# Kernel optimization log

Hardware: AMD Instinct MI355X
Metric: run time of the kernel (lower is better)

## Reference

```python
import jax, jax.numpy as jnp
import numpy as np

WS = (8, 8)   # window size
SS = (4, 4)   # shift size
NH = 3        # num heads


def _attn_mask(pad_H, pad_W):
    """Standard Swin shifted-window attention mask, shape (nW, L, L)."""
    img = np.zeros((pad_H, pad_W), dtype=np.int32)
    cnt = 0
    for hs in (slice(0, -WS[0]), slice(-WS[0], -SS[0]), slice(-SS[0], None)):
        for ws_ in (slice(0, -WS[1]), slice(-WS[1], -SS[1]), slice(-SS[1], None)):
            img[hs, ws_] = cnt
            cnt += 1
    nH, nW = pad_H // WS[0], pad_W // WS[1]
    m = img.reshape(nH, WS[0], nW, WS[1]).transpose(0, 2, 1, 3).reshape(nH * nW, WS[0] * WS[1])
    diff = m[:, None, :] - m[:, :, None]
    return jnp.asarray(np.where(diff != 0, -100.0, 0.0).astype(np.float32))


def setup_inputs() -> dict:
    key = jax.random.key(0)
    ks = jax.random.split(key, 6)
    B, H, W, C = 16, 128, 128, 96
    L = WS[0] * WS[1]
    return {
        "x": jax.random.normal(ks[0], (B, H, W, C), jnp.float32),
        "qkv_w": jax.random.normal(ks[1], (3 * C, C), jnp.float32) * 0.05,
        "qkv_b": jax.random.normal(ks[2], (3 * C,), jnp.float32) * 0.05,
        "proj_w": jax.random.normal(ks[3], (C, C), jnp.float32) * 0.05,
        "proj_b": jax.random.normal(ks[4], (C,), jnp.float32) * 0.05,
        "rel_bias": jax.random.normal(ks[5], (NH, L, L), jnp.float32) * 0.05,
    }


def reference(x, qkv_w, qkv_b, proj_w, proj_b, rel_bias):
    B, H, W, C = x.shape
    pad_b = (WS[0] - H % WS[0]) % WS[0]
    pad_r = (WS[1] - W % WS[1]) % WS[1]
    x = jnp.pad(x, ((0, 0), (0, pad_b), (0, pad_r), (0, 0)))
    pad_H, pad_W = H + pad_b, W + pad_r
    ss = [0 if WS[0] >= pad_H else SS[0], 0 if WS[1] >= pad_W else SS[1]]
    shifted = sum(ss) > 0
    if shifted:
        x = jnp.roll(x, (-ss[0], -ss[1]), axis=(1, 2))
    nH, nW = pad_H // WS[0], pad_W // WS[1]
    num_win = nH * nW
    L = WS[0] * WS[1]
    d = C // NH
    # window partition -> (B*nW, L, C)
    xw = x.reshape(B, nH, WS[0], nW, WS[1], C).transpose(0, 1, 3, 2, 4, 5)
    xw = xw.reshape(B * num_win, L, C)
    # qkv projection
    qkv = xw @ qkv_w.T + qkv_b                       # (BnW, L, 3C)
    qkv = qkv.reshape(B * num_win, L, 3, NH, d).transpose(2, 0, 3, 1, 4)
    q, k, v = qkv[0], qkv[1], qkv[2]                 # (BnW, NH, L, d)
    q = q * (d ** -0.5)
    attn = jnp.einsum("whqd,whkd->whqk", q, k)       # (BnW, NH, L, L)
    attn = attn + rel_bias[None]
    if shifted:
        mask = _attn_mask(pad_H, pad_W)              # (nW, L, L)
        attn = attn.reshape(B, num_win, NH, L, L) + mask[None, :, None]
        attn = attn.reshape(B * num_win, NH, L, L)
    attn = jax.nn.softmax(attn, axis=-1)
    out = jnp.einsum("whqk,whkd->whqd", attn, v)     # (BnW, NH, L, d)
    out = out.transpose(0, 2, 1, 3).reshape(B * num_win, L, C)
    out = out @ proj_w.T + proj_b
    # un-window
    out = out.reshape(B, nH, nW, WS[0], WS[1], C).transpose(0, 1, 3, 2, 4, 5)
    out = out.reshape(B, pad_H, pad_W, C)
    if shifted:
        out = jnp.roll(out, (ss[0], ss[1]), axis=(1, 2))
    return out[:, :H, :W, :]
```

## Files before the change

kernel.cpp:

```cpp
#include <hip/hip_runtime.h>
#include <hip/hip_bf16.h>


typedef __attribute__((ext_vector_type(8))) short short8;
typedef __attribute__((ext_vector_type(4))) float f32x4;

#define XST 104
#define VST 72

#define WS_QKVW 0
#define WS_PROJW 27648
#define WS_QKVB_BYTES 73728
#define WS_PROJB_BYTES 74880
#define WS_BIAST_BYTES 75776
#define WS_TOTAL_BYTES (WS_BIAST_BYTES + 3 * 32 * 64 * 4)

#define INV_LN2 1.4426950408889634f
#define MASK_NEG 144.26950408889634f

__device__ __forceinline__ unsigned short f2b(float f) {
    union { float f; unsigned u; } v; v.f = f;
    unsigned r = v.u + 0x7fffu + ((v.u >> 16) & 1u);
    return (unsigned short)(r >> 16);
}

__device__ __forceinline__ unsigned pk2(float a, float b) {
    union { __hip_bfloat162 h; unsigned u; } z;
    z.h = __float22bfloat162_rn(make_float2(a, b));
    return z.u;
}
__device__ __forceinline__ float blo(unsigned u) {
    union { unsigned u; float f; } z; z.u = u << 16; return z.f;
}
__device__ __forceinline__ float bhi(unsigned u) {
    union { unsigned u; float f; } z; z.u = u & 0xffff0000u; return z.f;
}

__global__ void prep_weights(const float* __restrict__ qkv_w,
                             const float* __restrict__ qkv_b,
                             const float* __restrict__ proj_w,
                             const float* __restrict__ proj_b,
                             const float* __restrict__ rel_bias,
                             void* __restrict__ ws, int do_bias)
{
    unsigned short* wsh = (unsigned short*)ws;
    float* fqb = (float*)((char*)ws + WS_QKVB_BYTES);
    float* fpb = (float*)((char*)ws + WS_PROJB_BYTES);
    unsigned* fb2 = (unsigned*)((char*)ws + WS_BIAST_BYTES);
    const float qs = 0.17677669529663687f * INV_LN2;

    int idx = blockIdx.x * 256 + threadIdx.x;
    if (idx < 27648) {
        int col = idx / 96;
        float v = qkv_w[idx];
        if (col < 96) v *= qs;
        wsh[WS_QKVW + idx] = f2b(v);
    } else if (idx < 36864) {
        wsh[WS_PROJW + (idx - 27648)] = f2b(proj_w[idx - 27648]);
    } else if (idx < 37152) {
        int col = idx - 36864;
        float v = qkv_b[col];
        if (col < 96) v *= qs;
        fqb[col] = v;
    } else if (idx < 37248) {
        fpb[idx - 37152] = proj_b[idx - 37152];
    } else if (do_bias && idx < 43392) {
        int i2 = idx - 37248;
        int h = i2 >> 11;
        int rem = i2 & 2047;
        int kp = rem >> 6, q = rem & 63;
        float lo = rel_bias[(h * 64 + q) * 64 + 2 * kp]     * INV_LN2;
        float hi = rel_bias[(h * 64 + q) * 64 + 2 * kp + 1] * INV_LN2;
        fb2[i2] = pk2(lo, hi);
    }
}

__global__ __launch_bounds__(256, 4) void swin_mfma(
    const float* __restrict__ x,
    const float* __restrict__ rel_bias,
    const unsigned* __restrict__ bias2,
    const void* __restrict__ ws,
    float* __restrict__ out)
{
    const unsigned short* wqkv  = (const unsigned short*)ws + WS_QKVW;
    const unsigned short* wproj = (const unsigned short*)ws + WS_PROJW;
    const float* wqkvb = (const float*)((const char*)ws + WS_QKVB_BYTES);
    const float* wprjb = (const float*)((const char*)ws + WS_PROJB_BYTES);

    __shared__ __align__(16) unsigned short xs[64 * XST];
    __shared__ __align__(16) unsigned short kb[3 * 64 * 32];
    __shared__ __align__(16) unsigned short vt[3 * 32 * VST];

    const int t    = threadIdx.x;
    const int wv   = t >> 6;
    const int lane = t & 63;
    const int quad = lane >> 4;
    const int l16  = lane & 15;
    const int m0   = wv * 16;

    const int blk = blockIdx.x;
    const int bb  = blk >> 8;
    const int win = blk & 255;
    const int wh  = win >> 4, ww = win & 15;

    for (int idx = t; idx < 1536; idx += 256) {
        int row = idx / 24;
        int c4  = idx - row * 24;
        int r = row >> 3, c = row & 7;
        int gh = (wh * 8 + r + 4) & 127;
        int gw = (ww * 8 + c + 4) & 127;
        float4 v = *(const float4*)&x[(((bb * 128 + gh) * 128 + gw) * 96) + c4 * 4];
        union { unsigned u[2]; ushort4 s; } pk;
        pk.u[0] = pk2(v.x, v.y);
        pk.u[1] = pk2(v.z, v.w);
        *(ushort4*)&xs[row * XST + c4 * 4] = pk.s;
    }
    __syncthreads();

    short8 af[4][3];
    #pragma unroll
    for (int mt = 0; mt < 4; ++mt)
        #pragma unroll
        for (int ks = 0; ks < 3; ++ks)
            af[mt][ks] = *(const short8*)&xs[(mt * 16 + l16) * XST + ks * 32 + quad * 8];
    __syncthreads();

    for (int nt = wv; nt < 18; nt += 4) {
        const int n0 = nt * 16;
        float bias = wqkvb[n0 + l16];
        f32x4 acc[4];
        #pragma unroll
        for (int mt = 0; mt < 4; ++mt) acc[mt] = (f32x4){bias, bias, bias, bias};
        #pragma unroll
        for (int ks = 0; ks < 3; ++ks) {
            short8 bf = *(const short8*)&wqkv[(n0 + l16) * 96 + ks * 32 + quad * 8];
            #pragma unroll
            for (int mt = 0; mt < 4; ++mt)
                acc[mt] = __builtin_amdgcn_mfma_f32_16x16x32_bf16(af[mt][ks], bf, acc[mt], 0, 0, 0);
        }
        if (nt < 6) {
            int col = n0 + l16;
            #pragma unroll
            for (int mt = 0; mt < 4; ++mt) {
                unsigned u01 = pk2(acc[mt][0], acc[mt][1]);
                unsigned u23 = pk2(acc[mt][2], acc[mt][3]);
                int rb = (mt * 16 + quad * 4) * XST + col;
                xs[rb]           = (unsigned short)u01;
                xs[rb + XST]     = (unsigned short)(u01 >> 16);
                xs[rb + 2 * XST] = (unsigned short)u23;
                xs[rb + 3 * XST] = (unsigned short)(u23 >> 16);
            }
        } else if (nt < 12) {
            int col = n0 - 96 + l16; int hh = col >> 5; int d = col & 31;
            int dch = d >> 3, dlo = d & 7;
            #pragma unroll
            for (int mt = 0; mt < 4; ++mt) {
                int base = hh * 64 + 32 * (mt >> 1) + 16 * (quad & 1)
                         + 8 * (mt & 1) + 4 * (quad >> 1);
                unsigned u01 = pk2(acc[mt][0], acc[mt][1]);
                unsigned u23 = pk2(acc[mt][2], acc[mt][3]);
                int c01 = ((dch ^ ((base >> 1) & 3)) << 3) + dlo;
                int c23 = ((dch ^ (((base >> 1) + 1) & 3)) << 3) + dlo;
                kb[(base + 0) * 32 + c01] = (unsigned short)u01;
                kb[(base + 1) * 32 + c01] = (unsigned short)(u01 >> 16);
                kb[(base + 2) * 32 + c23] = (unsigned short)u23;
                kb[(base + 3) * 32 + c23] = (unsigned short)(u23 >> 16);
            }
        } else {
            int col = n0 - 192 + l16; int hh = col >> 5; int d = col & 31;
            #pragma unroll
            for (int mt = 0; mt < 4; ++mt) {
                union { unsigned u[2]; ushort4 s; } pk;
                pk.u[0] = pk2(acc[mt][0], acc[mt][1]);
                pk.u[1] = pk2(acc[mt][2], acc[mt][3]);
                *(ushort4*)&vt[(hh * 32 + d) * VST + mt * 16 + quad * 4] = pk.s;
            }
        }
    }
    __syncthreads();

    {
        const bool bh = (wh == 15), bw = (ww == 15);
        const bool edge = bh || bw;
        const int qtok = m0 + l16;
        const int qrr = bh ? (((qtok >> 3) < 4) ? 1 : 2) : 0;
        const int qcc = bw ? (((qtok & 7) < 4) ? 1 : 2) : 0;

        auto qkhead = [&](f32x4* s, int h) {
            short8 qa = *(const short8*)&xs[(m0 + l16) * XST + h * 32 + quad * 8];
            #pragma unroll
            for (int nt = 0; nt < 4; ++nt) {
                int k0 = 32 * (nt >> 1) + 8 * quad + 4 * (nt & 1);
                float bv[4];
                if (bias2) {
                    int kpb = k0 >> 1;
                    unsigned u0 = bias2[(h * 32 + kpb) * 64 + qtok];
                    unsigned u1 = bias2[(h * 32 + kpb + 1) * 64 + qtok];
                    bv[0] = blo(u0); bv[1] = bhi(u0);
                    bv[2] = blo(u1); bv[3] = bhi(u1);
                } else {
                    #pragma unroll
                    for (int r = 0; r < 4; ++r)
                        bv[r] = rel_bias[(h * 64 + qtok) * 64 + k0 + r] * INV_LN2;
                }
                f32x4 z;
                if (edge) {
                    #pragma unroll
                    for (int r = 0; r < 4; ++r) {
                        int ktok = k0 + r;
                        int krr = bh ? (((ktok >> 3) < 4) ? 1 : 2) : 0;
                        int kcc = bw ? (((ktok & 7) < 4) ? 1 : 2) : 0;
                        z[r] = bv[r] - ((krr != qrr || kcc != qcc) ? MASK_NEG : 0.f);
                    }
                } else {
                    z[0] = bv[0]; z[1] = bv[1]; z[2] = bv[2]; z[3] = bv[3];
                }
                int rowk = h * 64 + nt * 16 + l16;
                short8 kf = *(const short8*)&kb[rowk * 32 + ((quad ^ ((rowk >> 1) & 3)) << 3)];
                s[nt] = __builtin_amdgcn_mfma_f32_16x16x32_bf16(kf, qa, z, 0, 0, 0);
            }
        };

        auto softpv = [&](f32x4* s, int h) {
            float p[4][4];
            float rs = 0.f;
            #pragma unroll
            for (int nt = 0; nt < 4; ++nt) {
                #pragma unroll
                for (int r = 0; r < 4; ++r) {
                    float e = exp2f(s[nt][r]);
                    p[nt][r] = e;
                    rs += e;
                }
            }
            rs += __shfl_xor(rs, 16);
            rs += __shfl_xor(rs, 32);
            float rinv = 1.0f / rs;

            short8 pa[2];
            #pragma unroll
            for (int kk = 0; kk < 2; ++kk) {
                union { unsigned u[4]; short8 s8; } uw;
                uw.u[0] = pk2(p[2 * kk][0] * rinv,     p[2 * kk][1] * rinv);
                uw.u[1] = pk2(p[2 * kk][2] * rinv,     p[2 * kk][3] * rinv);
                uw.u[2] = pk2(p[2 * kk + 1][0] * rinv, p[2 * kk + 1][1] * rinv);
                uw.u[3] = pk2(p[2 * kk + 1][2] * rinv, p[2 * kk + 1][3] * rinv);
                pa[kk] = uw.s8;
            }

            f32x4 o0 = (f32x4){0.f, 0.f, 0.f, 0.f};
            f32x4 o1 = o0;
            #pragma unroll
            for (int kk = 0; kk < 2; ++kk) {
                short8 v0 = *(const short8*)&vt[(h * 32 + l16) * VST + kk * 32 + quad * 8];
                short8 v1 = *(const short8*)&vt[(h * 32 + 16 + l16) * VST + kk * 32 + quad * 8];
                o0 = __builtin_amdgcn_mfma_f32_16x16x32_bf16(pa[kk], v0, o0, 0, 0, 0);
                o1 = __builtin_amdgcn_mfma_f32_16x16x32_bf16(pa[kk], v1, o1, 0, 0, 0);
            }
            int ob = (m0 + quad * 4) * XST + h * 32 + l16;
            unsigned a01 = pk2(o0[0], o0[1]);
            unsigned a23 = pk2(o0[2], o0[3]);
            unsigned b01 = pk2(o1[0], o1[1]);
            unsigned b23 = pk2(o1[2], o1[3]);
            xs[ob]                = (unsigned short)a01;
            xs[ob + XST]          = (unsigned short)(a01 >> 16);
            xs[ob + 2 * XST]      = (unsigned short)a23;
            xs[ob + 3 * XST]      = (unsigned short)(a23 >> 16);
            xs[ob + 16]           = (unsigned short)b01;
            xs[ob + XST + 16]     = (unsigned short)(b01 >> 16);
            xs[ob + 2 * XST + 16] = (unsigned short)b23;
            xs[ob + 3 * XST + 16] = (unsigned short)(b23 >> 16);
        };

        f32x4 sA[4], sB[4], sC[4];
        qkhead(sA, 0);
        qkhead(sB, 1);
        softpv(sA, 0);
        qkhead(sC, 2);
        softpv(sB, 1);
        softpv(sC, 2);
    }

    {
        short8 pja[3];
        #pragma unroll
        for (int ks = 0; ks < 3; ++ks)
            pja[ks] = *(const short8*)&xs[(m0 + l16) * XST + ks * 32 + quad * 8];

        int rowbase[4];
        #pragma unroll
        for (int r = 0; r < 4; ++r) {
            int tok = m0 + quad * 4 + r;
            int tr = tok >> 3, tc = tok & 7;
            int gh = (wh * 8 + tr + 4) & 127;
            int gw = (ww * 8 + tc + 4) & 127;
            rowbase[r] = ((bb * 128 + gh) * 128 + gw) * 96;
        }
        #pragma unroll
        for (int nt = 0; nt < 6; ++nt) {
            const int n0 = nt * 16;
            float bias = wprjb[n0 + l16];
            f32x4 acc = (f32x4){bias, bias, bias, bias};
            #pragma unroll
            for (int ks = 0; ks < 3; ++ks) {
                short8 bf = *(const short8*)&wproj[(n0 + l16) * 96 + ks * 32 + quad * 8];
                acc = __builtin_amdgcn_mfma_f32_16x16x32_bf16(pja[ks], bf, acc, 0, 0, 0);
            }
            #pragma unroll
            for (int r = 0; r < 4; ++r)
                out[rowbase[r] + n0 + l16] = acc[r];
        }
    }
}

extern "C" void kernel_launch(void* const* d_in, const int* in_sizes, int n_in,
                              void* d_out, int out_size, void* d_ws, size_t ws_size,
                              hipStream_t stream) {
    const float* x        = (const float*)d_in[0];
    const float* qkv_w    = (const float*)d_in[1];
    const float* qkv_b    = (const float*)d_in[2];
    const float* proj_w   = (const float*)d_in[3];
    const float* proj_b   = (const float*)d_in[4];
    const float* rel_bias = (const float*)d_in[5];
    float* out = (float*)d_out;

    const unsigned* bias2 = nullptr;
    if (ws_size >= (size_t)WS_TOTAL_BYTES)
        bias2 = (const unsigned*)((const char*)d_ws + WS_BIAST_BYTES);

    hipLaunchKernelGGL(prep_weights, dim3(170), dim3(256), 0, stream,
                       qkv_w, qkv_b, proj_w, proj_b, rel_bias, d_ws, bias2 ? 1 : 0);
    hipLaunchKernelGGL(swin_mfma, dim3(4096), dim3(256), 0, stream,
                       x, rel_bias, bias2, (const void*)d_ws, out);
}
```

Measured before the change: 236.9 us.

## Process attention heads sequentially to shrink LDS and raise occupancy

The QKV projection now runs one head at a time. Each wave computes the Q, K and V columns for its own 16 token rows, keeping only its slice of x in registers. K and V buffers in shared memory shrink to a single head, roughly halving LDS per block, and launch bounds move from 4 to 6 blocks per CU. In exchange, every wave now reads the full QKV weight matrix instead of a quarter of it, and the schedule gains extra block barriers between heads. It also loses the earlier interleaving of QK and softmax across heads.

Measured after the change: 259.1 us. 9.4% more time.

```diff
diff --git a/kernel.cpp b/kernel.cpp
--- a/kernel.cpp
+++ b/kernel.cpp
@@ -75,7 +75,7 @@
     }
 }
 
-__global__ __launch_bounds__(256, 4) void swin_mfma(
+__global__ __launch_bounds__(256, 6) void swin_mfma(
     const float* __restrict__ x,
     const float* __restrict__ rel_bias,
     const unsigned* __restrict__ bias2,
@@ -88,8 +88,8 @@
     const float* wprjb = (const float*)((const char*)ws + WS_PROJB_BYTES);
 
     __shared__ __align__(16) unsigned short xs[64 * XST];
-    __shared__ __align__(16) unsigned short kb[3 * 64 * 32];
-    __shared__ __align__(16) unsigned short vt[3 * 32 * VST];
+    __shared__ __align__(16) unsigned short kb[64 * 32];
+    __shared__ __align__(16) unsigned short vt[32 * VST];
 
     const int t    = threadIdx.x;
     const int wv   = t >> 6;
@@ -117,77 +117,71 @@
     }
     __syncthreads();
 
-    short8 af[4][3];
+    short8 af[3];
     #pragma unroll
-    for (int mt = 0; mt < 4; ++mt)
-        #pragma unroll
-        for (int ks = 0; ks < 3; ++ks)
-            af[mt][ks] = *(const short8*)&xs[(mt * 16 + l16) * XST + ks * 32 + quad * 8];
-    __syncthreads();
-
-    for (int nt = wv; nt < 18; nt += 4) {
-        const int n0 = nt * 16;
-        float bias = wqkvb[n0 + l16];
-        f32x4 acc[4];
-        #pragma unroll
-        for (int mt = 0; mt < 4; ++mt) acc[mt] = (f32x4){bias, bias, bias, bias};
+    for (int ks = 0; ks < 3; ++ks)
+        af[ks] = *(const short8*)&xs[(m0 + l16) * XST + ks * 32 + quad * 8];
+
+    auto gemm16 = [&](int n0) -> f32x4 {
+        float b = wqkvb[n0 + l16];
+        f32x4 acc = (f32x4){b, b, b, b};
         #pragma unroll
         for (int ks = 0; ks < 3; ++ks) {
             short8 bf = *(const short8*)&wqkv[(n0 + l16) * 96 + ks * 32 + quad * 8];
-            #pragma unroll
-            for (int mt = 0; mt < 4; ++mt)
-                acc[mt] = __builtin_amdgcn_mfma_f32_16x16x32_bf16(af[mt][ks], bf, acc[mt], 0, 0, 0);
-        }
-        if (nt < 6) {
-            int col = n0 + l16;
-            #pragma unroll
-            for (int mt = 0; mt < 4; ++mt) {
-                unsigned u01 = pk2(acc[mt][0], acc[mt][1]);
-                unsigned u23 = pk2(acc[mt][2], acc[mt][3]);
-                int rb = (mt * 16 + quad * 4) * XST + col;
-                xs[rb]           = (unsigned short)u01;
-                xs[rb + XST]     = (unsigned short)(u01 >> 16);
-                xs[rb + 2 * XST] = (unsigned short)u23;
-                xs[rb + 3 * XST] = (unsigned short)(u23 >> 16);
-            }
-        } else if (nt < 12) {
-            int col = n0 - 96 + l16; int hh = col >> 5; int d = col & 31;
+            acc = __builtin_amdgcn_mfma_f32_16x16x32_bf16(af[ks], bf, acc, 0, 0, 0);
+        }
+        return acc;
+    };
+
+    const int kbase = 32 * (wv >> 1) + 16 * (quad & 1) + 8 * (wv & 1) + 4 * (quad >> 1);
+
+    const bool bh = (wh == 15), bw = (ww == 15);
+    const bool edge = bh || bw;
+    const int qtok = m0 + l16;
+    const int qrr = bh ? (((qtok >> 3) < 4) ? 1 : 2) : 0;
+    const int qcc = bw ? (((qtok & 7) < 4) ? 1 : 2) : 0;
+
+    for (int h = 0; h < 3; ++h) {
+        #pragma unroll
+        for (int qi = 0; qi < 2; ++qi) {
+            int qt = 2 * h + qi;
+            f32x4 acc = gemm16(qt * 16);
+            unsigned u01 = pk2(acc[0], acc[1]);
+            unsigned u23 = pk2(acc[2], acc[3]);
+            int rb = (m0 + quad * 4) * XST + qt * 16 + l16;
+            xs[rb]           = (unsigned short)u01;
+            xs[rb + XST]     = (unsigned short)(u01 >> 16);
+            xs[rb + 2 * XST] = (unsigned short)u23;
+            xs[rb + 3 * XST] = (unsigned short)(u23 >> 16);
+        }
+        #pragma unroll
+        for (int half = 0; half < 2; ++half) {
+            f32x4 acc = gemm16(96 + h * 32 + half * 16);
+            int d = half * 16 + l16;
             int dch = d >> 3, dlo = d & 7;
-            #pragma unroll
-            for (int mt = 0; mt < 4; ++mt) {
-                int base = hh * 64 + 32 * (mt >> 1) + 16 * (quad & 1)
-                         + 8 * (mt & 1) + 4 * (quad >> 1);
-                unsigned u01 = pk2(acc[mt][0], acc[mt][1]);
-                unsigned u23 = pk2(acc[mt][2], acc[mt][3]);
-                int c01 = ((dch ^ ((base >> 1) & 3)) << 3) + dlo;
-                int c23 = ((dch ^ (((base >> 1) + 1) & 3)) << 3) + dlo;
-                kb[(base + 0) * 32 + c01] = (unsigned short)u01;
-                kb[(base + 1) * 32 + c01] = (unsigned short)(u01 >> 16);
-                kb[(base + 2) * 32 + c23] = (unsigned short)u23;
-                kb[(base + 3) * 32 + c23] = (unsigned short)(u23 >> 16);
-            }
-        } else {
-            int col = n0 - 192 + l16; int hh = col >> 5; int d = col & 31;
-            #pragma unroll
-            for (int mt = 0; mt < 4; ++mt) {
-                union { unsigned u[2]; ushort4 s; } pk;
-                pk.u[0] = pk2(acc[mt][0], acc[mt][1]);
-                pk.u[1] = pk2(acc[mt][2], acc[mt][3]);
-                *(ushort4*)&vt[(hh * 32 + d) * VST + mt * 16 + quad * 4] = pk.s;
-            }
-        }
-    }
-    __syncthreads();
-
-    {
-        const bool bh = (wh == 15), bw = (ww == 15);
-        const bool edge = bh || bw;
-        const int qtok = m0 + l16;
-        const int qrr = bh ? (((qtok >> 3) < 4) ? 1 : 2) : 0;
-        const int qcc = bw ? (((qtok & 7) < 4) ? 1 : 2) : 0;
-
-        auto qkhead = [&](f32x4* s, int h) {
+            unsigned u01 = pk2(acc[0], acc[1]);
+            unsigned u23 = pk2(acc[2], acc[3]);
+            int c01 = ((dch ^ ((kbase >> 1) & 3)) << 3) + dlo;
+            int c23 = ((dch ^ (((kbase >> 1) + 1) & 3)) << 3) + dlo;
+            kb[(kbase + 0) * 32 + c01] = (unsigned short)u01;
+            kb[(kbase + 1) * 32 + c01] = (unsigned short)(u01 >> 16);
+            kb[(kbase + 2) * 32 + c23] = (unsigned short)u23;
+            kb[(kbase + 3) * 32 + c23] = (unsigned short)(u23 >> 16);
+        }
+        #pragma unroll
+        for (int half = 0; half < 2; ++half) {
+            f32x4 acc = gemm16(192 + h * 32 + half * 16);
+            int d = half * 16 + l16;
+            union { unsigned u[2]; ushort4 s; } pk;
+            pk.u[0] = pk2(acc[0], acc[1]);
+            pk.u[1] = pk2(acc[2], acc[3]);
+            *(ushort4*)&vt[d * VST + m0 + quad * 4] = pk.s;
+        }
+        __syncthreads();
+
+        {
             short8 qa = *(const short8*)&xs[(m0 + l16) * XST + h * 32 + quad * 8];
+            f32x4 s[4];
             #pragma unroll
             for (int nt = 0; nt < 4; ++nt) {
                 int k0 = 32 * (nt >> 1) + 8 * quad + 4 * (nt & 1);
@@ -215,13 +209,10 @@
                 } else {
                     z[0] = bv[0]; z[1] = bv[1]; z[2] = bv[2]; z[3] = bv[3];
                 }
-                int rowk = h * 64 + nt * 16 + l16;
+                int rowk = nt * 16 + l16;
                 short8 kf = *(const short8*)&kb[rowk * 32 + ((quad ^ ((rowk >> 1) & 3)) << 3)];
                 s[nt] = __builtin_amdgcn_mfma_f32_16x16x32_bf16(kf, qa, z, 0, 0, 0);
             }
-        };
-
-        auto softpv = [&](f32x4* s, int h) {
             float p[4][4];
             float rs = 0.f;
             #pragma unroll
@@ -252,8 +243,8 @@
             f32x4 o1 = o0;
             #pragma unroll
             for (int kk = 0; kk < 2; ++kk) {
-                short8 v0 = *(const short8*)&vt[(h * 32 + l16) * VST + kk * 32 + quad * 8];
-                short8 v1 = *(const short8*)&vt[(h * 32 + 16 + l16) * VST + kk * 32 + quad * 8];
+                short8 v0 = *(const short8*)&vt[(l16) * VST + kk * 32 + quad * 8];
+                short8 v1 = *(const short8*)&vt[(16 + l16) * VST + kk * 32 + quad * 8];
                 o0 = __builtin_amdgcn_mfma_f32_16x16x32_bf16(pa[kk], v0, o0, 0, 0, 0);
                 o1 = __builtin_amdgcn_mfma_f32_16x16x32_bf16(pa[kk], v1, o1, 0, 0, 0);
             }
@@ -270,15 +261,8 @@
             xs[ob + XST + 16]     = (unsigned short)(b01 >> 16);
             xs[ob + 2 * XST + 16] = (unsigned short)b23;
             xs[ob + 3 * XST + 16] = (unsigned short)(b23 >> 16);
-        };
-
-        f32x4 sA[4], sB[4], sC[4];
-        qkhead(sA, 0);
-        qkhead(sB, 1);
-        softpv(sA, 0);
-        qkhead(sC, 2);
-        softpv(sB, 1);
-        softpv(sC, 2);
+        }
+        if (h < 2) __syncthreads();
     }
 
     {
```
